# Optimization experiments

Measured on AMD Instinct MI355X. Metric: run time of the kernel, lower is better.

## Reference

```python
import jax, jax.numpy as jnp
import numpy as np

VOCAB, EMB, HID = 50257, 256, 512
T, B = 512, 64


def setup_inputs() -> dict:
    key = jax.random.key(0)
    ks = jax.random.split(key, 9)
    x = jax.random.randint(ks[0], (T, B), 0, VOCAB)
    # pack_padded_sequence requires lengths sorted descending, each >= 1
    x_len = jnp.sort(jax.random.randint(ks[1], (B,), 1, T + 1))[::-1]
    s_e = 1.0 / np.sqrt(HID)
    emb = jax.random.normal(ks[2], (VOCAB, EMB), dtype=jnp.float32)
    W_ih = jax.random.uniform(ks[3], (4 * HID, EMB), minval=-s_e, maxval=s_e, dtype=jnp.float32)
    W_hh = jax.random.uniform(ks[4], (4 * HID, HID), minval=-s_e, maxval=s_e, dtype=jnp.float32)
    b_ih = jax.random.uniform(ks[5], (4 * HID,), minval=-s_e, maxval=s_e, dtype=jnp.float32)
    b_hh = jax.random.uniform(ks[6], (4 * HID,), minval=-s_e, maxval=s_e, dtype=jnp.float32)
    fc_w = jax.random.uniform(ks[7], (1, HID), minval=-s_e, maxval=s_e, dtype=jnp.float32)
    fc_b = jax.random.uniform(ks[8], (1,), minval=-s_e, maxval=s_e, dtype=jnp.float32)
    return {"x": x, "x_len": x_len, "emb": emb, "W_ih": W_ih, "W_hh": W_hh,
            "b_ih": b_ih, "b_hh": b_hh, "fc_w": fc_w, "fc_b": fc_b}


def _lstm_last_hidden(xe, x_len, W_ih, W_hh, b_ih, b_hh):
    # xe: [T, B, E]; packed-sequence semantics == freeze state once t >= len
    Tn, Bn, _ = xe.shape
    H = W_hh.shape[1]
    mask = (jnp.arange(Tn)[:, None] < x_len[None, :])[..., None]  # [T, B, 1]
    h0 = jnp.zeros((Bn, H), dtype=xe.dtype)
    c0 = jnp.zeros((Bn, H), dtype=xe.dtype)

    def step(carry, inp):
        h, c = carry
        xt, m = inp  # xt: [B, E], m: [B, 1]
        gates = xt @ W_ih.T + b_ih + h @ W_hh.T + b_hh  # [B, 4H]
        i, f, g, o = jnp.split(gates, 4, axis=-1)       # torch gate order i,f,g,o
        i = jax.nn.sigmoid(i)
        f = jax.nn.sigmoid(f)
        g = jnp.tanh(g)
        o = jax.nn.sigmoid(o)
        c_new = f * c + i * g
        h_new = o * jnp.tanh(c_new)
        h = jnp.where(m, h_new, h)
        c = jnp.where(m, c_new, c)
        return (h, c), None

    (h, _), _ = jax.lax.scan(step, (h0, c0), (xe, mask))
    return h  # [B, H] hidden at each sequence's last valid step


def reference(x, x_len, emb, W_ih, W_hh, b_ih, b_hh, fc_w, fc_b):
    xe = emb[x]  # [T, B, E] embedding gather
    h = _lstm_last_hidden(xe, x_len, W_ih, W_hh, b_ih, b_hh)
    logits = h @ fc_w.T + fc_b  # [B, 1]
    return jax.nn.sigmoid(logits)
```

## Files before the change

kernel.cpp:

```cpp
#include <hip/hip_runtime.h>

#define TT 512
#define BB 64
#define EE 256
#define HH 512
#define NWG 64
#define THREADS 256

typedef unsigned short u16;
typedef unsigned int u32;
typedef unsigned long long u64;
typedef __attribute__((ext_vector_type(8))) short bh8;
typedef __attribute__((ext_vector_type(4))) float f32x4;

__device__ __forceinline__ u16 f2b(float f) {
  union { float f; u32 u; } v; v.f = f;
  return (u16)((v.u + 0x7fffu + ((v.u >> 16) & 1u)) >> 16);
}
__device__ __forceinline__ float b2f(u16 b) {
  union { u32 u; float f; } v; v.u = ((u32)b) << 16; return v.f;
}
__device__ __forceinline__ float sigm(float x) { return 1.f / (1.f + __expf(-x)); }
__device__ __forceinline__ float tanh_f(float x) {
  float e = __expf(2.f * x);
  return 1.f - 2.f / (e + 1.f);
}

__global__ void k_init(u32* __restrict__ z) {
  const int gid = blockIdx.x * 256 + threadIdx.x;
  if (gid < 40960) z[gid] = 0u;
}

__global__ __launch_bounds__(256) void k_embed(const int* __restrict__ x,
    const float* __restrict__ emb, u16* __restrict__ xe)
{
  const int gid = blockIdx.x * 256 + threadIdx.x;
  const int tb  = gid >> 5;
  const int e0  = (gid & 31) << 3;
  const int tok = x[tb];
  const float4* s = (const float4*)(emb + (size_t)tok * EE + e0);
  float4 a = s[0], b = s[1];
  u16 o[8] = { f2b(a.x), f2b(a.y), f2b(a.z), f2b(a.w),
               f2b(b.x), f2b(b.y), f2b(b.z), f2b(b.w) };
  *(uint4*)(xe + (size_t)tb * EE + e0) = *(uint4*)o;
}

__global__ __launch_bounds__(THREADS, 1) void k_lstm(
    const float* __restrict__ Whh, const float* __restrict__ Wih,
    const float* __restrict__ bih, const float* __restrict__ bhh,
    const u16* __restrict__ xe, const int* __restrict__ xlen,
    u16* __restrict__ hbuf, u32* __restrict__ flags)
{
  __shared__ u16 lWhh[32 * HH];
  __shared__ u16 lWih[32 * EE];

  const int wg   = blockIdx.x;
  const int tid  = threadIdx.x;
  const int wave = tid >> 6;
  const int lane = tid & 63;
  const int n16  = lane & 15;
  const int grp  = lane >> 4;

  #pragma unroll
  for (int it = 0; it < 8; ++it) {
    int idx = it * THREADS + tid;
    int n   = idx >> 6;
    int c0  = (idx & 63) << 3;
    int grow = (n >> 3) * HH + wg * 8 + (n & 7);
    const float* s = Whh + (size_t)grow * HH + c0;
    u16 tmp[8];
    #pragma unroll
    for (int j = 0; j < 8; ++j) tmp[j] = f2b(s[j]);
    *(uint4*)((char*)lWhh + (u32)(n * 1024 + ((c0 << 1) ^ ((n & 7) << 4)))) = *(uint4*)tmp;
  }
  #pragma unroll
  for (int it = 0; it < 4; ++it) {
    int idx = it * THREADS + tid;
    int n   = idx >> 5;
    int c0  = (idx & 31) << 3;
    int grow = (n >> 3) * HH + wg * 8 + (n & 7);
    const float* s = Wih + (size_t)grow * EE + c0;
    u16 tmp[8];
    #pragma unroll
    for (int j = 0; j < 8; ++j) tmp[j] = f2b(s[j]);
    *(uint4*)((char*)lWih + (u32)(n * 512 + ((c0 << 1) ^ ((n & 7) << 4)))) = *(uint4*)tmp;
  }

  const int r0 = (n16 < 8) ? (wg * 8 + n16) : (HH + wg * 8 + (n16 - 8));
  const int r1 = (n16 < 8) ? (2 * HH + wg * 8 + n16) : (3 * HH + wg * 8 + (n16 - 8));
  const float bs0 = bih[r0] + bhh[r0];
  const float bs1 = bih[r1] + bhh[r1];

  int   lenr[4];
  int   mrow[4];
  float cst[4] = {0.f, 0.f, 0.f, 0.f};
  float hst[4] = {0.f, 0.f, 0.f, 0.f};
  #pragma unroll
  for (int r = 0; r < 4; ++r) { mrow[r] = wave * 16 + grp * 4 + r; lenr[r] = xlen[mrow[r]]; }
  int wmax = lenr[0];
  #pragma unroll
  for (int r = 1; r < 4; ++r) wmax = max(wmax, lenr[r]);
  #pragma unroll
  for (int off = 1; off < 64; off <<= 1) wmax = max(wmax, __shfl_xor(wmax, off));

  const int  arow = wave * 16 + n16;
  const u32  swz  = (u32)((n16 & 7) << 4);
  const char* pWhh0 = (const char*)lWhh + n16 * 1024;
  const char* pWhh1 = (const char*)lWhh + (16 + n16) * 1024;
  const char* pWih0 = (const char*)lWih + n16 * 512;
  const char* pWih1 = (const char*)lWih + (16 + n16) * 512;

  u32* myf = flags + (size_t)(wg * 4 + wave) * 32;
  u32* pf  = flags + (size_t)(lane * 4 + wave) * 32;

  __syncthreads();

  for (int t = 0; t < TT; ++t) {
    if (t > wmax) break;

    bh8 xf[8];
    {
      const u16* px = xe + ((size_t)t * BB + arow) * EE + grp * 8;
      #pragma unroll
      for (int k = 0; k < 8; ++k) xf[k] = *(const bh8*)(px + k * 32);
    }

    if (t > 0) {
      u32 v;
      do {
        v = __hip_atomic_load(pf, __ATOMIC_RELAXED, __HIP_MEMORY_SCOPE_AGENT);
      } while (v < (u32)t);
      asm volatile("" ::: "memory");
    }

    const u16* ph = hbuf + (size_t)(t & 1) * (BB * HH) + (size_t)arow * HH + grp * 8;
    bh8 hf[16];
    #pragma unroll
    for (int k = 0; k < 16; ++k) {
      union { u64 u[2]; bh8 v; } c;
      u64* p = (u64*)(ph + k * 32);
      c.u[0] = __hip_atomic_load(p,     __ATOMIC_RELAXED, __HIP_MEMORY_SCOPE_AGENT);
      c.u[1] = __hip_atomic_load(p + 1, __ATOMIC_RELAXED, __HIP_MEMORY_SCOPE_AGENT);
      hf[k] = c.v;
    }

    f32x4 acc0 = {bs0, bs0, bs0, bs0};
    f32x4 acc1 = {bs1, bs1, bs1, bs1};
    #pragma unroll
    for (int k = 0; k < 8; ++k) {
      const u32 o = ((u32)(k * 64 + grp * 16)) ^ swz;
      bh8 b0 = *(const bh8*)(pWih0 + o);
      bh8 b1 = *(const bh8*)(pWih1 + o);
      acc0 = __builtin_amdgcn_mfma_f32_16x16x32_bf16(xf[k], b0, acc0, 0, 0, 0);
      acc1 = __builtin_amdgcn_mfma_f32_16x16x32_bf16(xf[k], b1, acc1, 0, 0, 0);
    }
    #pragma unroll
    for (int k = 0; k < 16; ++k) {
      const u32 o = ((u32)(k * 64 + grp * 16)) ^ swz;
      bh8 b0 = *(const bh8*)(pWhh0 + o);
      bh8 b1 = *(const bh8*)(pWhh1 + o);
      acc0 = __builtin_amdgcn_mfma_f32_16x16x32_bf16(hf[k], b0, acc0, 0, 0, 0);
      acc1 = __builtin_amdgcn_mfma_f32_16x16x32_bf16(hf[k], b1, acc1, 0, 0, 0);
    }

    u16* hw = hbuf + (size_t)((t & 1) ^ 1) * (BB * HH);
    #pragma unroll
    for (int r = 0; r < 4; ++r) {
      const float v0 = acc0[r];
      const float v1 = acc1[r];
      const float fv = __shfl_xor(v0, 8);
      const float ov = __shfl_xor(v1, 8);
      const float iv = sigm(v0);
      const float ff = sigm(fv);
      const float gv = tanh_f(v1);
      const float oo = sigm(ov);
      const float cn = ff * cst[r] + iv * gv;
      const float hn = oo * tanh_f(cn);
      const bool valid = (t < lenr[r]);
      cst[r] = valid ? cn : cst[r];
      hst[r] = valid ? hn : hst[r];
      u32 hv = (u32)f2b(hst[r]);
      u32 up = __shfl_xor(hv, 1);
      if (((n16 & 1) == 0) && (n16 < 8) && (t <= lenr[r]))
        __hip_atomic_store((u32*)(hw + (size_t)mrow[r] * HH + wg * 8 + n16),
                           hv | (up << 16), __ATOMIC_RELAXED, __HIP_MEMORY_SCOPE_AGENT);
    }

    asm volatile("s_waitcnt vmcnt(0)" ::: "memory");
    if (lane == 0)
      __hip_atomic_store(myf, (u32)(t + 1), __ATOMIC_RELAXED, __HIP_MEMORY_SCOPE_AGENT);
  }

  asm volatile("s_waitcnt vmcnt(0)" ::: "memory");
  if (lane == 0)
    __hip_atomic_store(myf, (u32)(TT + 1), __ATOMIC_RELAXED, __HIP_MEMORY_SCOPE_AGENT);
}

__global__ __launch_bounds__(64) void k_fc(const u16* __restrict__ h0,
    const float* __restrict__ fcw, const float* __restrict__ fcb,
    float* __restrict__ out)
{
  const int b = blockIdx.x;
  const int lane = threadIdx.x;
  const u16* hr = h0 + (size_t)b * HH;
  float s = 0.f;
  #pragma unroll
  for (int j = 0; j < 8; ++j) {
    const int u = lane + j * 64;
    s += b2f(hr[u]) * fcw[u];
  }
  #pragma unroll
  for (int off = 32; off > 0; off >>= 1) s += __shfl_xor(s, off);
  if (lane == 0) out[b] = sigm(s + fcb[0]);
}

extern "C" void kernel_launch(void* const* d_in, const int* in_sizes, int n_in,
                              void* d_out, int out_size, void* d_ws, size_t ws_size,
                              hipStream_t stream)
{
  const int*   x    = (const int*)  d_in[0];
  const int*   xlen = (const int*)  d_in[1];
  const float* emb  = (const float*)d_in[2];
  const float* Wih  = (const float*)d_in[3];
  const float* Whh  = (const float*)d_in[4];
  const float* bih  = (const float*)d_in[5];
  const float* bhh  = (const float*)d_in[6];
  const float* fcw  = (const float*)d_in[7];
  const float* fcb  = (const float*)d_in[8];
  float* out = (float*)d_out;

  char* ws = (char*)d_ws;
  u16* xe    = (u16*)ws;
  u16* hbuf  = (u16*)(ws + (size_t)TT * BB * EE * 2);
  u32* flags = (u32*)(ws + (size_t)TT * BB * EE * 2 + (size_t)2 * BB * HH * 2);

  k_init <<<dim3(160), dim3(256), 0, stream>>>((u32*)hbuf);
  k_embed<<<dim3((TT * BB * EE / 8) / 256), dim3(256), 0, stream>>>(x, emb, xe);
  k_lstm <<<dim3(NWG), dim3(THREADS), 0, stream>>>(Whh, Wih, bih, bhh, xe, xlen, hbuf, flags);
  k_fc   <<<dim3(BB), dim3(64), 0, stream>>>(hbuf, fcw, fcb, out);
}
```

Before: 2.234 ms.

## Store full per-step hidden history and overlap x-projection with flag wait

When the workspace is large enough, hidden states go to a per-timestep buffer instead of a double buffer. Each step then reads a fresh address, so plain cached loads replace the slow per-element atomic loads, and the final layer reads h at each sequence's length. The input-projection MFMAs move ahead of the spin-wait, and the next step's embeddings are prefetched. The flag layout is compacted into contiguous words per wave. Correctness now leans on cache behaviour for never-before-read addresses, and the fallback path uses sc0 sc1 loads with an explicit waitcnt.

```diff
diff --git a/kernel.cpp b/kernel.cpp
--- a/kernel.cpp
+++ b/kernel.cpp
@@ -6,6 +6,7 @@
 #define HH 512
 #define NWG 64
 #define THREADS 256
+#define BBHH (BB * HH)
 
 typedef unsigned short u16;
 typedef unsigned int u32;
@@ -26,9 +27,11 @@
   return 1.f - 2.f / (e + 1.f);
 }
 
-__global__ void k_init(u32* __restrict__ z) {
+
+__global__ void k_init(u32* __restrict__ flags, u32* __restrict__ hb) {
   const int gid = blockIdx.x * 256 + threadIdx.x;
-  if (gid < 40960) z[gid] = 0u;
+  if (gid < 1024) flags[gid] = 0u;
+  if (gid < 32768) hb[gid] = 0u;
 }
 
 __global__ __launch_bounds__(256) void k_embed(const int* __restrict__ x,
@@ -45,6 +48,7 @@
   *(uint4*)(xe + (size_t)tb * EE + e0) = *(uint4*)o;
 }
 
+template<bool CACHED>
 __global__ __launch_bounds__(THREADS, 1) void k_lstm(
     const float* __restrict__ Whh, const float* __restrict__ Wih,
     const float* __restrict__ bih, const float* __restrict__ bhh,
@@ -110,19 +114,30 @@
   const char* pWih0 = (const char*)lWih + n16 * 512;
   const char* pWih1 = (const char*)lWih + (16 + n16) * 512;
 
-  u32* myf = flags + (size_t)(wg * 4 + wave) * 32;
-  u32* pf  = flags + (size_t)(lane * 4 + wave) * 32;
+  u32* myf = flags + wave * 64 + wg;
+  u32* pf  = flags + wave * 64 + lane;
 
   __syncthreads();
+
+  bh8 xf[8];
+  {
+    const u16* px = xe + (size_t)arow * EE + grp * 8;
+    #pragma unroll
+    for (int k = 0; k < 8; ++k) xf[k] = *(const bh8*)(px + k * 32);
+  }
 
   for (int t = 0; t < TT; ++t) {
     if (t > wmax) break;
 
-    bh8 xf[8];
-    {
-      const u16* px = xe + ((size_t)t * BB + arow) * EE + grp * 8;
-      #pragma unroll
-      for (int k = 0; k < 8; ++k) xf[k] = *(const bh8*)(px + k * 32);
+    f32x4 acc0 = {bs0, bs0, bs0, bs0};
+    f32x4 acc1 = {bs1, bs1, bs1, bs1};
+    #pragma unroll
+    for (int k = 0; k < 8; ++k) {
+      const u32 o = ((u32)(k * 64 + grp * 16)) ^ swz;
+      bh8 b0 = *(const bh8*)(pWih0 + o);
+      bh8 b1 = *(const bh8*)(pWih1 + o);
+      acc0 = __builtin_amdgcn_mfma_f32_16x16x32_bf16(xf[k], b0, acc0, 0, 0, 0);
+      acc1 = __builtin_amdgcn_mfma_f32_16x16x32_bf16(xf[k], b1, acc1, 0, 0, 0);
     }
 
     if (t > 0) {
@@ -133,27 +148,34 @@
       asm volatile("" ::: "memory");
     }
 
-    const u16* ph = hbuf + (size_t)(t & 1) * (BB * HH) + (size_t)arow * HH + grp * 8;
+    const u16* ph = (CACHED ? hbuf + (size_t)t * BBHH
+                            : hbuf + (size_t)(t & 1) * BBHH)
+                    + (size_t)arow * HH + grp * 8;
     bh8 hf[16];
-    #pragma unroll
-    for (int k = 0; k < 16; ++k) {
-      union { u64 u[2]; bh8 v; } c;
-      u64* p = (u64*)(ph + k * 32);
-      c.u[0] = __hip_atomic_load(p,     __ATOMIC_RELAXED, __HIP_MEMORY_SCOPE_AGENT);
-      c.u[1] = __hip_atomic_load(p + 1, __ATOMIC_RELAXED, __HIP_MEMORY_SCOPE_AGENT);
-      hf[k] = c.v;
-    }
-
-    f32x4 acc0 = {bs0, bs0, bs0, bs0};
-    f32x4 acc1 = {bs1, bs1, bs1, bs1};
-    #pragma unroll
-    for (int k = 0; k < 8; ++k) {
-      const u32 o = ((u32)(k * 64 + grp * 16)) ^ swz;
-      bh8 b0 = *(const bh8*)(pWih0 + o);
-      bh8 b1 = *(const bh8*)(pWih1 + o);
-      acc0 = __builtin_amdgcn_mfma_f32_16x16x32_bf16(xf[k], b0, acc0, 0, 0, 0);
-      acc1 = __builtin_amdgcn_mfma_f32_16x16x32_bf16(xf[k], b1, acc1, 0, 0, 0);
-    }
+    if (CACHED) {
+      #pragma unroll
+      for (int k = 0; k < 16; ++k) hf[k] = *(const bh8*)(ph + k * 32);
+    } else {
+      #pragma unroll
+      for (int k = 0; k < 16; ++k) {
+        const u16* pk = ph + k * 32;
+        asm volatile("global_load_dwordx4 %0, %1, off sc0 sc1"
+                     : "=v"(hf[k]) : "v"(pk) : "memory");
+      }
+    }
+
+    {
+      const int tn = (t + 1 < TT) ? t + 1 : t;
+      const u16* px = xe + ((size_t)tn * BB + arow) * EE + grp * 8;
+      #pragma unroll
+      for (int k = 0; k < 8; ++k) xf[k] = *(const bh8*)(px + k * 32);
+    }
+
+    if (!CACHED) {
+      asm volatile("s_waitcnt vmcnt(0)" ::: "memory");
+      __builtin_amdgcn_sched_barrier(0);
+    }
+
     #pragma unroll
     for (int k = 0; k < 16; ++k) {
       const u32 o = ((u32)(k * 64 + grp * 16)) ^ swz;
@@ -163,7 +185,8 @@
       acc1 = __builtin_amdgcn_mfma_f32_16x16x32_bf16(hf[k], b1, acc1, 0, 0, 0);
     }
 
-    u16* hw = hbuf + (size_t)((t & 1) ^ 1) * (BB * HH);
+    u16* hw = CACHED ? hbuf + (size_t)(t + 1) * BBHH
+                     : hbuf + (size_t)((t & 1) ^ 1) * BBHH;
     #pragma unroll
     for (int r = 0; r < 4; ++r) {
       const float v0 = acc0[r];
@@ -181,7 +204,8 @@
       hst[r] = valid ? hn : hst[r];
       u32 hv = (u32)f2b(hst[r]);
       u32 up = __shfl_xor(hv, 1);
-      if (((n16 & 1) == 0) && (n16 < 8) && (t <= lenr[r]))
+      const bool dost = CACHED ? valid : (t <= lenr[r]);
+      if (((n16 & 1) == 0) && (n16 < 8) && dost)
         __hip_atomic_store((u32*)(hw + (size_t)mrow[r] * HH + wg * 8 + n16),
                            hv | (up << 16), __ATOMIC_RELAXED, __HIP_MEMORY_SCOPE_AGENT);
     }
@@ -196,13 +220,13 @@
     __hip_atomic_store(myf, (u32)(TT + 1), __ATOMIC_RELAXED, __HIP_MEMORY_SCOPE_AGENT);
 }
 
-__global__ __launch_bounds__(64) void k_fc(const u16* __restrict__ h0,
-    const float* __restrict__ fcw, const float* __restrict__ fcb,
-    float* __restrict__ out)
+__global__ __launch_bounds__(64) void k_fc(const u16* __restrict__ hbuf,
+    const int* __restrict__ xlen, const float* __restrict__ fcw,
+    const float* __restrict__ fcb, float* __restrict__ out, int mode)
 {
   const int b = blockIdx.x;
   const int lane = threadIdx.x;
-  const u16* hr = h0 + (size_t)b * HH;
+  const u16* hr = hbuf + (mode ? (size_t)xlen[b] * BBHH : (size_t)0) + (size_t)b * HH;
   float s = 0.f;
   #pragma unroll
   for (int j = 0; j < 8; ++j) {
@@ -230,12 +254,19 @@
   float* out = (float*)d_out;
 
   char* ws = (char*)d_ws;
-  u16* xe    = (u16*)ws;
-  u16* hbuf  = (u16*)(ws + (size_t)TT * BB * EE * 2);
-  u32* flags = (u32*)(ws + (size_t)TT * BB * EE * 2 + (size_t)2 * BB * HH * 2);
-
-  k_init <<<dim3(160), dim3(256), 0, stream>>>((u32*)hbuf);
+  u32* flags = (u32*)ws;
+  u16* xe    = (u16*)(ws + 4096);
+  u16* hbuf  = (u16*)(ws + 4096 + (size_t)TT * BB * EE * 2);
+
+  const bool cached = (ws_size >= (size_t)50401280);
+
+  k_init <<<dim3(128), dim3(256), 0, stream>>>(flags, (u32*)hbuf);
   k_embed<<<dim3((TT * BB * EE / 8) / 256), dim3(256), 0, stream>>>(x, emb, xe);
-  k_lstm <<<dim3(NWG), dim3(THREADS), 0, stream>>>(Whh, Wih, bih, bhh, xe, xlen, hbuf, flags);
-  k_fc   <<<dim3(BB), dim3(64), 0, stream>>>(hbuf, fcw, fcb, out);
-}
+  if (cached) {
+    k_lstm<true> <<<dim3(NWG), dim3(THREADS), 0, stream>>>(Whh, Wih, bih, bhh, xe, xlen, hbuf, flags);
+    k_fc<<<dim3(BB), dim3(64), 0, stream>>>(hbuf, xlen, fcw, fcb, out, 1);
+  } else {
+    k_lstm<false><<<dim3(NWG), dim3(THREADS), 0, stream>>>(Whh, Wih, bih, bhh, xe, xlen, hbuf, flags);
+    k_fc<<<dim3(BB), dim3(64), 0, stream>>>(hbuf, xlen, fcw, fcb, out, 0);
+  }
+}
```

Measured after the change: 2.701 ms. 1.21x slower.

## Run an independent LSTM replica per XCD with XCD-local h exchange and flags

Applied to the files above, without the earlier changes.

Launches 256 workgroups that register per XCD at startup. If each XCD holds exactly 32, every XCD runs a full redundant LSTM replica whose h-exchange buffer and flags stay XCD-local, read and written with sc0-only cache bits. Otherwise it falls back to a global mode where only 32 workgroups run and the rest exit. Each workgroup now owns 16 hidden units across all four gates, keeps W_ih in registers and W_hh in dynamic LDS, and prefetches the next step's x during the recurrence. The aim is to cut cross-XCD coherence latency on the per-step barrier, at the cost of redundant compute and a fragile startup handshake.

```diff
diff --git a/kernel.cpp b/kernel.cpp
--- a/kernel.cpp
+++ b/kernel.cpp
@@ -4,8 +4,18 @@
 #define BB 64
 #define EE 256
 #define HH 512
-#define NWG 64
+#define NWG 256
 #define THREADS 256
+#define BBHH (BB * HH)
+
+#define WS_REG      0u
+#define WS_FLAGSL   64u
+#define WS_FLAGSG   4160u
+#define WS_HBUFL    65536u
+#define WS_HBUFG    1114112u
+#define WS_HOUT     1245184u
+#define WS_XE       1310720u
+#define WS_ZERO_U32 311296u
 
 typedef unsigned short u16;
 typedef unsigned int u32;
@@ -26,9 +36,28 @@
   return 1.f - 2.f / (e + 1.f);
 }
 
+__device__ __forceinline__ bh8 ldh(const u16* p, bool loc) {
+  bh8 v;
+  if (loc) asm volatile("global_load_dwordx4 %0, %1, off sc0"     : "=v"(v) : "v"(p));
+  else     asm volatile("global_load_dwordx4 %0, %1, off sc0 sc1" : "=v"(v) : "v"(p));
+  return v;
+}
+__device__ __forceinline__ void st32(u32* p, u32 v, bool loc) {
+  if (loc) asm volatile("global_store_dword %0, %1, off sc0"     :: "v"(p), "v"(v) : "memory");
+  else     asm volatile("global_store_dword %0, %1, off sc0 sc1" :: "v"(p), "v"(v) : "memory");
+}
+__device__ __forceinline__ u32 ldf(const u32* p, bool loc) {
+  u32 v;
+  if (loc) asm volatile("global_load_dword %0, %1, off sc0\n\ts_waitcnt vmcnt(0)"
+                        : "=v"(v) : "v"(p) : "memory");
+  else     asm volatile("global_load_dword %0, %1, off sc0 sc1\n\ts_waitcnt vmcnt(0)"
+                        : "=v"(v) : "v"(p) : "memory");
+  return v;
+}
+
 __global__ void k_init(u32* __restrict__ z) {
-  const int gid = blockIdx.x * 256 + threadIdx.x;
-  if (gid < 40960) z[gid] = 0u;
+  const u32 gid = blockIdx.x * 256 + threadIdx.x;
+  if (gid < WS_ZERO_U32) z[gid] = 0u;
 }
 
 __global__ __launch_bounds__(256) void k_embed(const int* __restrict__ x,
@@ -49,160 +78,202 @@
     const float* __restrict__ Whh, const float* __restrict__ Wih,
     const float* __restrict__ bih, const float* __restrict__ bhh,
     const u16* __restrict__ xe, const int* __restrict__ xlen,
-    u16* __restrict__ hbuf, u32* __restrict__ flags)
+    u32* regp, u32* flagsL, u32* flagsG, u16* hbufL, u16* hbufG,
+    u16* hout)
 {
-  __shared__ u16 lWhh[32 * HH];
-  __shared__ u16 lWih[32 * EE];
-
-  const int wg   = blockIdx.x;
+  extern __shared__ u16 lWhh[];
+
   const int tid  = threadIdx.x;
   const int wave = tid >> 6;
   const int lane = tid & 63;
   const int n16  = lane & 15;
   const int grp  = lane >> 4;
 
-  #pragma unroll
-  for (int it = 0; it < 8; ++it) {
+  __shared__ u32 sh[4];
+  if (tid == 0) {
+    u32 xcd;
+    asm volatile("s_getreg_b32 %0, hwreg(HW_REG_XCC_ID)" : "=s"(xcd));
+    xcd &= 7u;
+    u32 sx = __hip_atomic_fetch_add(&regp[1 + xcd], 1u, __ATOMIC_RELAXED, __HIP_MEMORY_SCOPE_AGENT);
+    asm volatile("s_waitcnt vmcnt(0)" ::: "memory");
+    u32 gs = __hip_atomic_fetch_add(&regp[0], 1u, __ATOMIC_RELAXED, __HIP_MEMORY_SCOPE_AGENT);
+    asm volatile("s_waitcnt vmcnt(0)" ::: "memory");
+    u64 t0; asm volatile("s_memtime %0" : "=s"(t0));
+    bool timeout = false;
+    while (__hip_atomic_load(&regp[0], __ATOMIC_RELAXED, __HIP_MEMORY_SCOPE_AGENT) < (u32)NWG) {
+      u64 tn; asm volatile("s_memtime %0" : "=s"(tn));
+      if (tn - t0 > 100000000ull) { timeout = true; break; }
+      __builtin_amdgcn_s_sleep(1);
+    }
+    u32 propose = 2u;
+    if (!timeout) {
+      bool ok = true;
+      #pragma unroll
+      for (int j = 0; j < 8; ++j)
+        ok &= (__hip_atomic_load(&regp[1 + j], __ATOMIC_RELAXED, __HIP_MEMORY_SCOPE_AGENT) == (u32)(NWG / 8));
+      propose = ok ? 1u : 2u;
+    }
+    u32 expd = 0u;
+    bool won = __hip_atomic_compare_exchange_strong(&regp[9], &expd, propose,
+                   __ATOMIC_RELAXED, __ATOMIC_RELAXED, __HIP_MEMORY_SCOPE_AGENT);
+    u32 mode = won ? propose : expd;
+    if (mode == 1u && timeout) {
+      while (__hip_atomic_load(&regp[0], __ATOMIC_RELAXED, __HIP_MEMORY_SCOPE_AGENT) < (u32)NWG)
+        __builtin_amdgcn_s_sleep(1);
+    }
+    sh[0] = (mode == 1u) ? sx : gs;
+    sh[1] = mode;
+    sh[2] = xcd;
+  }
+  __syncthreads();
+  const u32  slot  = sh[0];
+  const bool local = (sh[1] == 1u);
+  const u32  xcd   = sh[2];
+  if (!local && slot >= 32u) return;
+
+  bh8 wihf[32];
+  #pragma unroll
+  for (int q = 0; q < 4; ++q) {
+    #pragma unroll
+    for (int kk = 0; kk < 8; ++kk) {
+      const float4* s = (const float4*)(Wih + (size_t)(q * HH + slot * 16 + n16) * EE + kk * 32 + grp * 8);
+      float4 a = s[0], b = s[1];
+      u16 tmp[8] = { f2b(a.x), f2b(a.y), f2b(a.z), f2b(a.w),
+                     f2b(b.x), f2b(b.y), f2b(b.z), f2b(b.w) };
+      wihf[q * 8 + kk] = *(bh8*)tmp;
+    }
+  }
+
+  #pragma unroll
+  for (int it = 0; it < 16; ++it) {
     int idx = it * THREADS + tid;
     int n   = idx >> 6;
     int c0  = (idx & 63) << 3;
-    int grow = (n >> 3) * HH + wg * 8 + (n & 7);
-    const float* s = Whh + (size_t)grow * HH + c0;
-    u16 tmp[8];
-    #pragma unroll
-    for (int j = 0; j < 8; ++j) tmp[j] = f2b(s[j]);
+    int grow = (n >> 4) * HH + slot * 16 + (n & 15);
+    const float4* s = (const float4*)(Whh + (size_t)grow * HH + c0);
+    float4 a = s[0], b = s[1];
+    u16 tmp[8] = { f2b(a.x), f2b(a.y), f2b(a.z), f2b(a.w),
+                   f2b(b.x), f2b(b.y), f2b(b.z), f2b(b.w) };
     *(uint4*)((char*)lWhh + (u32)(n * 1024 + ((c0 << 1) ^ ((n & 7) << 4)))) = *(uint4*)tmp;
   }
-  #pragma unroll
-  for (int it = 0; it < 4; ++it) {
-    int idx = it * THREADS + tid;
-    int n   = idx >> 5;
-    int c0  = (idx & 31) << 3;
-    int grow = (n >> 3) * HH + wg * 8 + (n & 7);
-    const float* s = Wih + (size_t)grow * EE + c0;
-    u16 tmp[8];
-    #pragma unroll
-    for (int j = 0; j < 8; ++j) tmp[j] = f2b(s[j]);
-    *(uint4*)((char*)lWih + (u32)(n * 512 + ((c0 << 1) ^ ((n & 7) << 4)))) = *(uint4*)tmp;
-  }
-
-  const int r0 = (n16 < 8) ? (wg * 8 + n16) : (HH + wg * 8 + (n16 - 8));
-  const int r1 = (n16 < 8) ? (2 * HH + wg * 8 + n16) : (3 * HH + wg * 8 + (n16 - 8));
-  const float bs0 = bih[r0] + bhh[r0];
-  const float bs1 = bih[r1] + bhh[r1];
+
+  float bsq[4];
+  #pragma unroll
+  for (int q = 0; q < 4; ++q)
+    bsq[q] = bih[q * HH + slot * 16 + n16] + bhh[q * HH + slot * 16 + n16];
 
   int   lenr[4];
-  int   mrow[4];
   float cst[4] = {0.f, 0.f, 0.f, 0.f};
   float hst[4] = {0.f, 0.f, 0.f, 0.f};
   #pragma unroll
-  for (int r = 0; r < 4; ++r) { mrow[r] = wave * 16 + grp * 4 + r; lenr[r] = xlen[mrow[r]]; }
+  for (int j = 0; j < 4; ++j) lenr[j] = xlen[wave * 16 + grp * 4 + j];
   int wmax = lenr[0];
   #pragma unroll
-  for (int r = 1; r < 4; ++r) wmax = max(wmax, lenr[r]);
+  for (int j = 1; j < 4; ++j) wmax = max(wmax, lenr[j]);
   #pragma unroll
   for (int off = 1; off < 64; off <<= 1) wmax = max(wmax, __shfl_xor(wmax, off));
 
-  const int  arow = wave * 16 + n16;
-  const u32  swz  = (u32)((n16 & 7) << 4);
-  const char* pWhh0 = (const char*)lWhh + n16 * 1024;
-  const char* pWhh1 = (const char*)lWhh + (16 + n16) * 1024;
-  const char* pWih0 = (const char*)lWih + n16 * 512;
-  const char* pWih1 = (const char*)lWih + (16 + n16) * 512;
-
-  u32* myf = flags + (size_t)(wg * 4 + wave) * 32;
-  u32* pf  = flags + (size_t)(lane * 4 + wave) * 32;
+  const int arow = wave * 16 + n16;
+  const u32 swz  = (u32)((n16 & 7) << 4);
+
+  u16* hb = local ? hbufL + (size_t)xcd * 2 * BBHH : hbufG;
+  u32* fb = local ? flagsL + (xcd * 4 + wave) * 32 : flagsG + wave * 32;
+  u32* myf = fb + slot;
+  const u32* pollp = fb + (lane & 31);
 
   __syncthreads();
+
+  bh8 xf[8];
+  {
+    const u16* px = xe + (size_t)arow * EE + grp * 8;
+    #pragma unroll
+    for (int k = 0; k < 8; ++k) xf[k] = *(const bh8*)(px + k * 32);
+  }
 
   for (int t = 0; t < TT; ++t) {
     if (t > wmax) break;
 
-    bh8 xf[8];
+    f32x4 acc[4];
+    #pragma unroll
+    for (int q = 0; q < 4; ++q) acc[q] = (f32x4){bsq[q], bsq[q], bsq[q], bsq[q]};
+    #pragma unroll
+    for (int kk = 0; kk < 8; ++kk) {
+      #pragma unroll
+      for (int q = 0; q < 4; ++q)
+        acc[q] = __builtin_amdgcn_mfma_f32_16x16x32_bf16(xf[kk], wihf[q * 8 + kk], acc[q], 0, 0, 0);
+    }
+
+    if (t > 0) {
+      u32 v;
+      do { v = ldf(pollp, local); } while (v < (u32)t);
+    }
+
+    const u16* ph = hb + (size_t)(t & 1) * BBHH + (size_t)arow * HH + grp * 8;
+    bh8 hf[16];
+    #pragma unroll
+    for (int k = 0; k < 16; ++k) hf[k] = ldh(ph + k * 32, local);
+    asm volatile("s_waitcnt vmcnt(0)" ::: "memory");
+    __builtin_amdgcn_sched_barrier(0);
+
     {
-      const u16* px = xe + ((size_t)t * BB + arow) * EE + grp * 8;
+      const int tn = (t + 1 < TT) ? t + 1 : t;
+      const u16* px = xe + ((size_t)tn * BB + arow) * EE + grp * 8;
       #pragma unroll
       for (int k = 0; k < 8; ++k) xf[k] = *(const bh8*)(px + k * 32);
     }
 
-    if (t > 0) {
-      u32 v;
-      do {
-        v = __hip_atomic_load(pf, __ATOMIC_RELAXED, __HIP_MEMORY_SCOPE_AGENT);
-      } while (v < (u32)t);
-      asm volatile("" ::: "memory");
-    }
-
-    const u16* ph = hbuf + (size_t)(t & 1) * (BB * HH) + (size_t)arow * HH + grp * 8;
-    bh8 hf[16];
-    #pragma unroll
-    for (int k = 0; k < 16; ++k) {
-      union { u64 u[2]; bh8 v; } c;
-      u64* p = (u64*)(ph + k * 32);
-      c.u[0] = __hip_atomic_load(p,     __ATOMIC_RELAXED, __HIP_MEMORY_SCOPE_AGENT);
-      c.u[1] = __hip_atomic_load(p + 1, __ATOMIC_RELAXED, __HIP_MEMORY_SCOPE_AGENT);
-      hf[k] = c.v;
-    }
-
-    f32x4 acc0 = {bs0, bs0, bs0, bs0};
-    f32x4 acc1 = {bs1, bs1, bs1, bs1};
-    #pragma unroll
-    for (int k = 0; k < 8; ++k) {
-      const u32 o = ((u32)(k * 64 + grp * 16)) ^ swz;
-      bh8 b0 = *(const bh8*)(pWih0 + o);
-      bh8 b1 = *(const bh8*)(pWih1 + o);
-      acc0 = __builtin_amdgcn_mfma_f32_16x16x32_bf16(xf[k], b0, acc0, 0, 0, 0);
-      acc1 = __builtin_amdgcn_mfma_f32_16x16x32_bf16(xf[k], b1, acc1, 0, 0, 0);
-    }
-    #pragma unroll
-    for (int k = 0; k < 16; ++k) {
-      const u32 o = ((u32)(k * 64 + grp * 16)) ^ swz;
-      bh8 b0 = *(const bh8*)(pWhh0 + o);
-      bh8 b1 = *(const bh8*)(pWhh1 + o);
-      acc0 = __builtin_amdgcn_mfma_f32_16x16x32_bf16(hf[k], b0, acc0, 0, 0, 0);
-      acc1 = __builtin_amdgcn_mfma_f32_16x16x32_bf16(hf[k], b1, acc1, 0, 0, 0);
-    }
-
-    u16* hw = hbuf + (size_t)((t & 1) ^ 1) * (BB * HH);
-    #pragma unroll
-    for (int r = 0; r < 4; ++r) {
-      const float v0 = acc0[r];
-      const float v1 = acc1[r];
-      const float fv = __shfl_xor(v0, 8);
-      const float ov = __shfl_xor(v1, 8);
-      const float iv = sigm(v0);
-      const float ff = sigm(fv);
-      const float gv = tanh_f(v1);
-      const float oo = sigm(ov);
-      const float cn = ff * cst[r] + iv * gv;
+    #pragma unroll
+    for (int kk = 0; kk < 16; ++kk) {
+      const u32 o = ((u32)(kk * 64 + grp * 16)) ^ swz;
+      #pragma unroll
+      for (int q = 0; q < 4; ++q) {
+        bh8 b = *(const bh8*)((const char*)lWhh + (u32)((q * 16 + n16) * 1024) + o);
+        acc[q] = __builtin_amdgcn_mfma_f32_16x16x32_bf16(hf[kk], b, acc[q], 0, 0, 0);
+      }
+    }
+
+    u16* hw = hb + (size_t)((t & 1) ^ 1) * BBHH;
+    #pragma unroll
+    for (int j = 0; j < 4; ++j) {
+      const int brow = wave * 16 + grp * 4 + j;
+      const float iv = sigm(acc[0][j]);
+      const float ff = sigm(acc[1][j]);
+      const float gv = tanh_f(acc[2][j]);
+      const float oo = sigm(acc[3][j]);
+      const float cn = ff * cst[j] + iv * gv;
       const float hn = oo * tanh_f(cn);
-      const bool valid = (t < lenr[r]);
-      cst[r] = valid ? cn : cst[r];
-      hst[r] = valid ? hn : hst[r];
-      u32 hv = (u32)f2b(hst[r]);
+      const bool valid = (t < lenr[j]);
+      cst[j] = valid ? cn : cst[j];
+      hst[j] = valid ? hn : hst[j];
+      u32 hv = (u32)f2b(hst[j]);
       u32 up = __shfl_xor(hv, 1);
-      if (((n16 & 1) == 0) && (n16 < 8) && (t <= lenr[r]))
-        __hip_atomic_store((u32*)(hw + (size_t)mrow[r] * HH + wg * 8 + n16),
-                           hv | (up << 16), __ATOMIC_RELAXED, __HIP_MEMORY_SCOPE_AGENT);
+      if (((n16 & 1) == 0) && (t <= lenr[j]))
+        st32((u32*)(hw + (size_t)brow * HH + slot * 16 + n16), hv | (up << 16), local);
     }
 
     asm volatile("s_waitcnt vmcnt(0)" ::: "memory");
-    if (lane == 0)
-      __hip_atomic_store(myf, (u32)(t + 1), __ATOMIC_RELAXED, __HIP_MEMORY_SCOPE_AGENT);
+    if (lane == 0) st32(myf, (u32)(t + 1), local);
   }
 
   asm volatile("s_waitcnt vmcnt(0)" ::: "memory");
-  if (lane == 0)
-    __hip_atomic_store(myf, (u32)(TT + 1), __ATOMIC_RELAXED, __HIP_MEMORY_SCOPE_AGENT);
-}
-
-__global__ __launch_bounds__(64) void k_fc(const u16* __restrict__ h0,
+  if (lane == 0) st32(myf, (u32)(TT + 1), local);
+  #pragma unroll
+  for (int j = 0; j < 4; ++j) {
+    const int brow = wave * 16 + grp * 4 + j;
+    u32 hv = (u32)f2b(hst[j]);
+    u32 up = __shfl_xor(hv, 1);
+    if ((n16 & 1) == 0)
+      *(u32*)(hout + (size_t)brow * HH + slot * 16 + n16) = hv | (up << 16);
+  }
+}
+
+__global__ __launch_bounds__(64) void k_fc(const u16* __restrict__ hout,
     const float* __restrict__ fcw, const float* __restrict__ fcb,
     float* __restrict__ out)
 {
   const int b = blockIdx.x;
   const int lane = threadIdx.x;
-  const u16* hr = h0 + (size_t)b * HH;
+  const u16* hr = hout + (size_t)b * HH;
   float s = 0.f;
   #pragma unroll
   for (int j = 0; j < 8; ++j) {
@@ -230,12 +301,20 @@
   float* out = (float*)d_out;
 
   char* ws = (char*)d_ws;
-  u16* xe    = (u16*)ws;
-  u16* hbuf  = (u16*)(ws + (size_t)TT * BB * EE * 2);
-  u32* flags = (u32*)(ws + (size_t)TT * BB * EE * 2 + (size_t)2 * BB * HH * 2);
-
-  k_init <<<dim3(160), dim3(256), 0, stream>>>((u32*)hbuf);
+  u32* regp   = (u32*)(ws + WS_REG);
+  u32* flagsL = (u32*)(ws + WS_FLAGSL);
+  u32* flagsG = (u32*)(ws + WS_FLAGSG);
+  u16* hbufL  = (u16*)(ws + WS_HBUFL);
+  u16* hbufG  = (u16*)(ws + WS_HBUFG);
+  u16* hout   = (u16*)(ws + WS_HOUT);
+  u16* xe     = (u16*)(ws + WS_XE);
+
+  (void)hipFuncSetAttribute((const void*)k_lstm,
+      hipFuncAttributeMaxDynamicSharedMemorySize, 98304);
+
+  k_init <<<dim3(1216), dim3(256), 0, stream>>>((u32*)ws);
   k_embed<<<dim3((TT * BB * EE / 8) / 256), dim3(256), 0, stream>>>(x, emb, xe);
-  k_lstm <<<dim3(NWG), dim3(THREADS), 0, stream>>>(Whh, Wih, bih, bhh, xe, xlen, hbuf, flags);
-  k_fc   <<<dim3(BB), dim3(64), 0, stream>>>(hbuf, fcw, fcb, out);
-}
+  k_lstm <<<dim3(NWG), dim3(THREADS), 98304, stream>>>(Whh, Wih, bih, bhh, xe, xlen,
+                                                       regp, flagsL, flagsG, hbufL, hbufG, hout);
+  k_fc   <<<dim3(BB), dim3(64), 0, stream>>>(hout, fcw, fcb, out);
+}
```

Measured after the change: 3.937 ms. +76.2%, slower.

## Pack step flags densely, use cache-bypassing loads, prefetch next input step

Applied to the files above, without the earlier changes.

Replaces the padded 32-bit per-wave flags with densely packed 16-bit flags, so each lane polls a contiguous 128-byte line per wave. The flag and h loads and stores now use inline asm with sc0 sc1 bits in place of HIP atomics. The input-projection MFMAs are moved ahead of the flag wait, and next-step embedding rows are prefetched while waiting, taking x loads off the critical path. The risk is that the 16-bit flags are correct only while values stay within range, and that the hand-written cache bits give the required cross-workgroup visibility.

```diff
diff --git a/kernel.cpp b/kernel.cpp
--- a/kernel.cpp
+++ b/kernel.cpp
@@ -6,6 +6,7 @@
 #define HH 512
 #define NWG 64
 #define THREADS 256
+#define BBHH (BB * HH)
 
 typedef unsigned short u16;
 typedef unsigned int u32;
@@ -26,9 +27,26 @@
   return 1.f - 2.f / (e + 1.f);
 }
 
-__global__ void k_init(u32* __restrict__ z) {
+__device__ __forceinline__ bh8 ldh16(const u16* p) {
+  bh8 v;
+  asm volatile("global_load_dwordx4 %0, %1, off sc0 sc1" : "=v"(v) : "v"(p));
+  return v;
+}
+__device__ __forceinline__ u32 ldf16(const u16* p) {
+  u32 v;
+  asm volatile("global_load_ushort %0, %1, off sc0 sc1\n\ts_waitcnt vmcnt(0)"
+               : "=v"(v) : "v"(p) : "memory");
+  return v;
+}
+__device__ __forceinline__ void stf16(u16* p, u32 v) {
+  asm volatile("global_store_short %0, %1, off sc0 sc1" :: "v"(p), "v"(v) : "memory");
+}
+
+
+__global__ void k_init(u32* __restrict__ flags, u32* __restrict__ hb) {
   const int gid = blockIdx.x * 256 + threadIdx.x;
-  if (gid < 40960) z[gid] = 0u;
+  if (gid < 1024) flags[gid] = 0u;
+  if (gid < 32768) hb[gid] = 0u;
 }
 
 __global__ __launch_bounds__(256) void k_embed(const int* __restrict__ x,
@@ -49,7 +67,7 @@
     const float* __restrict__ Whh, const float* __restrict__ Wih,
     const float* __restrict__ bih, const float* __restrict__ bhh,
     const u16* __restrict__ xe, const int* __restrict__ xlen,
-    u16* __restrict__ hbuf, u32* __restrict__ flags)
+    u16* __restrict__ hbuf, u16* __restrict__ flags)
 {
   __shared__ u16 lWhh[32 * HH];
   __shared__ u16 lWih[32 * EE];
@@ -110,39 +128,20 @@
   const char* pWih0 = (const char*)lWih + n16 * 512;
   const char* pWih1 = (const char*)lWih + (16 + n16) * 512;
 
-  u32* myf = flags + (size_t)(wg * 4 + wave) * 32;
-  u32* pf  = flags + (size_t)(lane * 4 + wave) * 32;
+  u16* myf = flags + wave * 64 + wg;
+  const u16* pf = flags + wave * 64 + lane;
 
   __syncthreads();
+
+  bh8 xf[8];
+  {
+    const u16* px = xe + (size_t)arow * EE + grp * 8;
+    #pragma unroll
+    for (int k = 0; k < 8; ++k) xf[k] = *(const bh8*)(px + k * 32);
+  }
 
   for (int t = 0; t < TT; ++t) {
     if (t > wmax) break;
-
-    bh8 xf[8];
-    {
-      const u16* px = xe + ((size_t)t * BB + arow) * EE + grp * 8;
-      #pragma unroll
-      for (int k = 0; k < 8; ++k) xf[k] = *(const bh8*)(px + k * 32);
-    }
-
-    if (t > 0) {
-      u32 v;
-      do {
-        v = __hip_atomic_load(pf, __ATOMIC_RELAXED, __HIP_MEMORY_SCOPE_AGENT);
-      } while (v < (u32)t);
-      asm volatile("" ::: "memory");
-    }
-
-    const u16* ph = hbuf + (size_t)(t & 1) * (BB * HH) + (size_t)arow * HH + grp * 8;
-    bh8 hf[16];
-    #pragma unroll
-    for (int k = 0; k < 16; ++k) {
-      union { u64 u[2]; bh8 v; } c;
-      u64* p = (u64*)(ph + k * 32);
-      c.u[0] = __hip_atomic_load(p,     __ATOMIC_RELAXED, __HIP_MEMORY_SCOPE_AGENT);
-      c.u[1] = __hip_atomic_load(p + 1, __ATOMIC_RELAXED, __HIP_MEMORY_SCOPE_AGENT);
-      hf[k] = c.v;
-    }
 
     f32x4 acc0 = {bs0, bs0, bs0, bs0};
     f32x4 acc1 = {bs1, bs1, bs1, bs1};
@@ -154,6 +153,27 @@
       acc0 = __builtin_amdgcn_mfma_f32_16x16x32_bf16(xf[k], b0, acc0, 0, 0, 0);
       acc1 = __builtin_amdgcn_mfma_f32_16x16x32_bf16(xf[k], b1, acc1, 0, 0, 0);
     }
+
+    if (t > 0) {
+      u32 v;
+      do { v = ldf16(pf); } while (v < (u32)t);
+      asm volatile("" ::: "memory");
+    }
+
+    const u16* ph = hbuf + (size_t)(t & 1) * BBHH + (size_t)arow * HH + grp * 8;
+    bh8 hf[16];
+    #pragma unroll
+    for (int k = 0; k < 16; ++k) hf[k] = ldh16(ph + k * 32);
+
+    {
+      const int tn = (t + 1 < TT) ? t + 1 : t;
+      const u16* px = xe + ((size_t)tn * BB + arow) * EE + grp * 8;
+      #pragma unroll
+      for (int k = 0; k < 8; ++k) xf[k] = *(const bh8*)(px + k * 32);
+    }
+    asm volatile("s_waitcnt vmcnt(0)" ::: "memory");
+    __builtin_amdgcn_sched_barrier(0);
+
     #pragma unroll
     for (int k = 0; k < 16; ++k) {
       const u32 o = ((u32)(k * 64 + grp * 16)) ^ swz;
@@ -163,7 +183,7 @@
       acc1 = __builtin_amdgcn_mfma_f32_16x16x32_bf16(hf[k], b1, acc1, 0, 0, 0);
     }
 
-    u16* hw = hbuf + (size_t)((t & 1) ^ 1) * (BB * HH);
+    u16* hw = hbuf + (size_t)((t & 1) ^ 1) * BBHH;
     #pragma unroll
     for (int r = 0; r < 4; ++r) {
       const float v0 = acc0[r];
@@ -187,13 +207,11 @@
     }
 
     asm volatile("s_waitcnt vmcnt(0)" ::: "memory");
-    if (lane == 0)
-      __hip_atomic_store(myf, (u32)(t + 1), __ATOMIC_RELAXED, __HIP_MEMORY_SCOPE_AGENT);
+    if (lane == 0) stf16(myf, (u32)(t + 1));
   }
 
   asm volatile("s_waitcnt vmcnt(0)" ::: "memory");
-  if (lane == 0)
-    __hip_atomic_store(myf, (u32)(TT + 1), __ATOMIC_RELAXED, __HIP_MEMORY_SCOPE_AGENT);
+  if (lane == 0) stf16(myf, (u32)(TT + 1));
 }
 
 __global__ __launch_bounds__(64) void k_fc(const u16* __restrict__ h0,
@@ -230,11 +248,11 @@
   float* out = (float*)d_out;
 
   char* ws = (char*)d_ws;
-  u16* xe    = (u16*)ws;
-  u16* hbuf  = (u16*)(ws + (size_t)TT * BB * EE * 2);
-  u32* flags = (u32*)(ws + (size_t)TT * BB * EE * 2 + (size_t)2 * BB * HH * 2);
-
-  k_init <<<dim3(160), dim3(256), 0, stream>>>((u32*)hbuf);
+  u16* flags = (u16*)ws;
+  u16* xe    = (u16*)(ws + 4096);
+  u16* hbuf  = (u16*)(ws + 4096 + (size_t)TT * BB * EE * 2);
+
+  k_init <<<dim3(128), dim3(256), 0, stream>>>((u32*)flags, (u32*)hbuf);
   k_embed<<<dim3((TT * BB * EE / 8) / 256), dim3(256), 0, stream>>>(x, emb, xe);
   k_lstm <<<dim3(NWG), dim3(THREADS), 0, stream>>>(Whh, Wih, bih, bhh, xe, xlen, hbuf, flags);
   k_fc   <<<dim3(BB), dim3(64), 0, stream>>>(hbuf, fcw, fcb, out);
```

Measured after the change: 2.855 ms. 27.8% more time.
